# Kernel tuning notes

Hardware: AMD Instinct MI355X
Metric: run time of the kernel (lower is better)

The kernel has to match this reference:

```python
import jax, jax.numpy as jnp
import numpy as np

E, B, F, L = 4, 8192, 2048, 100  # envs, batch/env, feature dim, num classes
LAM = 1.0  # hparams['RERM_lam']


def setup_inputs() -> dict:
    key = jax.random.key(0)
    k1, k2, k3 = jax.random.split(key, 3)
    feats = jax.random.normal(k1, (E, B, F), jnp.float32)
    y = jax.random.randint(k2, (E, B), 0, L)
    W = jax.random.normal(k3, (F, L), jnp.float32) * 0.02
    b = jnp.zeros((L,), jnp.float32)
    return {"feats": feats, "y": y, "W": W, "b": b}


def _rerm_loss(feats, y, W, b):
    # --- per-(label, env) masked means (mean_table / visit_table) ---
    onehot = jax.nn.one_hot(y, L, dtype=feats.dtype)          # [E,B,L]
    counts = onehot.sum(axis=1)                               # [E,L]
    sums = jnp.einsum('ebl,ebf->elf', onehot, feats)          # [E,L,F]
    means = sums / jnp.maximum(counts, 1.0)[..., None]        # [E,L,F]
    visit = (counts > 0).astype(feats.dtype)                  # [E,L]

    # --- torch.var(mean_table[i, fetch_envs, :], dim=1): variance over
    # feature dim per env (unbiased, /(F-1)), then mean over visited envs ---
    mu = means.mean(axis=-1, keepdims=True)                   # [E,L,1]
    var = jnp.sum((means - mu) ** 2, axis=-1) / (F - 1)       # [E,L]

    nvis = visit.sum(axis=0)                                  # [L]
    sel = (nvis > 1.5).astype(feats.dtype)                    # labels with >1 env
    per_label = (var * visit).sum(axis=0) / jnp.maximum(nvis, 1.0)  # [L]
    nzlabel = jnp.maximum(sel.sum(), 1.0)
    mean_loss = LAM * jnp.sum(per_label * sel) / nzlabel

    # --- cross-entropy over all envs concatenated ---
    logits = feats.reshape(E * B, F) @ W + b                  # [E*B,L]
    logp = jax.nn.log_softmax(logits, axis=-1)
    ce = -jnp.take_along_axis(logp, y.reshape(-1, 1), axis=1).mean()

    return mean_loss + ce


def reference(feats, y, W, b):
    return _rerm_loss(feats, y, W, b)
```

## Files before the change

kernel.cpp:

```cpp
#include <hip/hip_runtime.h>
#include <hip/hip_bf16.h>
#include <math.h>

#define E 4
#define B 8192
#define F 2048
#define L 100
#define NROWS (E * B)
#define LAMBDA 1.0f

typedef __attribute__((ext_vector_type(8))) short bf16x8;
typedef __attribute__((ext_vector_type(4))) float f32x4;

static __device__ inline unsigned short f2bf(float x) {
    unsigned u = __float_as_uint(x);
    unsigned r = (u + 0x7FFFu + ((u >> 16) & 1u)) >> 16;
    return (unsigned short)r;
}

#define SG 4
#define NSG 25
#define SBS 8
#define SRW (B / SBS)
#define NSUM (E * SBS * NSG)

#define GBM 128
#define GNC 112
#define GKC 64
#define APAD 72
#define NGEMM (NROWS / GBM)

__global__ void __launch_bounds__(256) k_prep(const float* __restrict__ W,
                                              unsigned short* __restrict__ Wt) {
    int g = blockIdx.x * 256 + threadIdx.x;
    int n = g >> 9;
    int k = (g & 511) * 4;
    ushort4 v;
    if (n < L) {
        v.x = f2bf(W[(size_t)(k + 0) * L + n]);
        v.y = f2bf(W[(size_t)(k + 1) * L + n]);
        v.z = f2bf(W[(size_t)(k + 2) * L + n]);
        v.w = f2bf(W[(size_t)(k + 3) * L + n]);
    } else {
        v.x = v.y = v.z = v.w = 0;
    }
    *(ushort4*)&Wt[(size_t)n * F + k] = v;
}

__global__ void __launch_bounds__(512, 4) k_main(const float* __restrict__ feats,
                                                 const int* __restrict__ y,
                                                 const unsigned short* __restrict__ Wt,
                                                 const float* __restrict__ bias,
                                                 float* __restrict__ partial,
                                                 int* __restrict__ counts,
                                                 float* __restrict__ ce_accum) {
    __shared__ __align__(16) char sm[34624];
    int t = threadIdx.x;

    if (blockIdx.x < NGEMM) {
        unsigned short* As = (unsigned short*)sm;
        unsigned short* Ws = As + GBM * APAD;
        float* red = (float*)(sm + 34560);
        int wave = t >> 6, lane = t & 63;
        int quad = lane >> 4, l16 = lane & 15;
        size_t row0 = (size_t)blockIdx.x * GBM;

        f32x4 acc[7];
#pragma unroll
        for (int ct = 0; ct < 7; ++ct) acc[ct] = (f32x4){0.f, 0.f, 0.f, 0.f};

        int srow = t >> 2;
        int sq = t & 3;

        const float* aptr = feats + (row0 + srow) * (size_t)F + sq * 16;
        const unsigned short* wptr = Wt + (size_t)srow * F + sq * 16;

        float4 pa[4];
        uint4 pw[2];
#pragma unroll
        for (int i = 0; i < 4; ++i) pa[i] = ((const float4*)aptr)[i];
        if (srow < GNC) {
#pragma unroll
            for (int i = 0; i < 2; ++i) pw[i] = ((const uint4*)wptr)[i];
        }

        for (int k0 = 0; k0 < F; k0 += GKC) {
            bf16x8 o0, o1;
            o0[0] = f2bf(pa[0].x); o0[1] = f2bf(pa[0].y); o0[2] = f2bf(pa[0].z); o0[3] = f2bf(pa[0].w);
            o0[4] = f2bf(pa[1].x); o0[5] = f2bf(pa[1].y); o0[6] = f2bf(pa[1].z); o0[7] = f2bf(pa[1].w);
            o1[0] = f2bf(pa[2].x); o1[1] = f2bf(pa[2].y); o1[2] = f2bf(pa[2].z); o1[3] = f2bf(pa[2].w);
            o1[4] = f2bf(pa[3].x); o1[5] = f2bf(pa[3].y); o1[6] = f2bf(pa[3].z); o1[7] = f2bf(pa[3].w);
            *(bf16x8*)&As[srow * APAD + sq * 16] = o0;
            *(bf16x8*)&As[srow * APAD + sq * 16 + 8] = o1;
            if (srow < GNC) {
                *(uint4*)&Ws[srow * APAD + sq * 16] = pw[0];
                *(uint4*)&Ws[srow * APAD + sq * 16 + 8] = pw[1];
            }
            __syncthreads();

            if (k0 + GKC < F) {
                const float* ap = aptr + k0 + GKC;
                const unsigned short* wp = wptr + k0 + GKC;
#pragma unroll
                for (int i = 0; i < 4; ++i) pa[i] = ((const float4*)ap)[i];
                if (srow < GNC) {
#pragma unroll
                    for (int i = 0; i < 2; ++i) pw[i] = ((const uint4*)wp)[i];
                }
            }

#pragma unroll
            for (int ks = 0; ks < 2; ++ks) {
                bf16x8 bfr = *(const bf16x8*)&As[(wave * 16 + l16) * APAD + ks * 32 + quad * 8];
#pragma unroll
                for (int ct = 0; ct < 7; ++ct) {
                    bf16x8 af = *(const bf16x8*)&Ws[(ct * 16 + l16) * APAD + ks * 32 + quad * 8];
                    acc[ct] = __builtin_amdgcn_mfma_f32_16x16x32_bf16(af, bfr, acc[ct], 0, 0, 0);
                }
            }
            __syncthreads();
        }

        int grow = (int)row0 + wave * 16 + l16;
        int lab = y[grow];
        float vv[7][4];
        float vm = -1e30f;
#pragma unroll
        for (int ct = 0; ct < 7; ++ct) {
#pragma unroll
            for (int r = 0; r < 4; ++r) {
                int c = ct * 16 + quad * 4 + r;
                float bb = (c < L) ? bias[c] : 0.f;
                float v = acc[ct][r] + bb;
                vv[ct][r] = v;
                if (c < L) vm = fmaxf(vm, v);
            }
        }
        vm = fmaxf(vm, __shfl_xor(vm, 16));
        vm = fmaxf(vm, __shfl_xor(vm, 32));
        float se = 0.f, tv = 0.f;
#pragma unroll
        for (int ct = 0; ct < 7; ++ct) {
#pragma unroll
            for (int r = 0; r < 4; ++r) {
                int c = ct * 16 + quad * 4 + r;
                if (c < L) se += __expf(vv[ct][r] - vm);
                if (c == lab) tv = vv[ct][r];
            }
        }
        se += __shfl_xor(se, 16);
        se += __shfl_xor(se, 32);
        tv += __shfl_xor(tv, 16);
        tv += __shfl_xor(tv, 32);
        float ce = vm + __logf(se) - tv;
#pragma unroll
        for (int s = 1; s <= 8; s <<= 1) ce += __shfl_xor(ce, s);
        if (lane == 0) red[wave] = ce;
        __syncthreads();
        if (t == 0) {
            float v = 0.f;
#pragma unroll
            for (int w = 0; w < 8; ++w) v += red[w];
            atomicAdd(ce_accum, v);
        }
    } else {
        int* ys = (int*)sm;
        unsigned short (*lists)[SRW] = (unsigned short (*)[SRW])(sm + 4096);
        int* cnt = (int*)(sm + 4096 + 8192);
        int bi = blockIdx.x - NGEMM;
        int lg = bi % NSG;
        int bs = (bi / NSG) % SBS;
        int e  = bi / (NSG * SBS);
        int lab0 = lg * SG;

        if (t < SG) cnt[t] = 0;
        const int* yb = y + e * B + bs * SRW;
        ys[t] = yb[t];
        ys[t + 512] = yb[t + 512];
        __syncthreads();

        for (int r = t; r < SRW; r += 512) {
            int lb = ys[r] - lab0;
            if ((unsigned)lb < SG) {
                int p = atomicAdd(&cnt[lb], 1);
                lists[lb][p] = (unsigned short)r;
            }
        }
        __syncthreads();

        const float* fb = feats + ((size_t)e * B + (size_t)bs * SRW) * F + t * 4;
#pragma unroll
        for (int lb = 0; lb < SG; ++lb) {
            int n = cnt[lb];
            float4 a0 = make_float4(0.f, 0.f, 0.f, 0.f);
            float4 a1 = make_float4(0.f, 0.f, 0.f, 0.f);
            int i = 0;
            for (; i + 2 <= n; i += 2) {
                int r0 = lists[lb][i];
                int r1 = lists[lb][i + 1];
                float4 x0 = *(const float4*)(fb + (size_t)r0 * F);
                float4 x1 = *(const float4*)(fb + (size_t)r1 * F);
                a0.x += x0.x; a0.y += x0.y; a0.z += x0.z; a0.w += x0.w;
                a1.x += x1.x; a1.y += x1.y; a1.z += x1.z; a1.w += x1.w;
            }
            if (i < n) {
                int r0 = lists[lb][i];
                float4 x0 = *(const float4*)(fb + (size_t)r0 * F);
                a0.x += x0.x; a0.y += x0.y; a0.z += x0.z; a0.w += x0.w;
            }
            float4 s;
            s.x = a0.x + a1.x; s.y = a0.y + a1.y;
            s.z = a0.z + a1.z; s.w = a0.w + a1.w;
            *(float4*)&partial[(((size_t)e * SBS + bs) * L + lab0 + lb) * F + t * 4] = s;
        }
        if (t < SG) atomicAdd(&counts[e * L + lab0 + t], cnt[t]);
    }
}

__global__ void k_var(const float* __restrict__ partial,
                      const int* __restrict__ counts,
                      float* __restrict__ var_out) {
    int el = blockIdx.x;
    int e = el / L, l = el % L;
    int t = threadIdx.x;
    float inv = 1.f / fmaxf((float)counts[el], 1.f);
    float sm = 0.f, sm2 = 0.f;
    for (int f = t; f < F; f += 256) {
        float s = 0.f;
#pragma unroll
        for (int bs = 0; bs < SBS; ++bs)
            s += partial[(((size_t)e * SBS + bs) * L + l) * F + f];
        float m = s * inv;
        sm += m; sm2 += m * m;
    }
    __shared__ float r1[256], r2[256];
    r1[t] = sm; r2[t] = sm2;
    __syncthreads();
    for (int s = 128; s > 0; s >>= 1) {
        if (t < s) { r1[t] += r1[t + s]; r2[t] += r2[t + s]; }
        __syncthreads();
    }
    if (t == 0) {
        float S = r1[0], S2 = r2[0];
        var_out[el] = (S2 - S * S / (float)F) / (float)(F - 1);
    }
}

__global__ void k_final(const int* __restrict__ counts,
                        const float* __restrict__ var_in,
                        const float* __restrict__ ce_accum,
                        float* __restrict__ out) {
    __shared__ float s_sum[128], s_cnt[128];
    int t = threadIdx.x;
    float selsum = 0.f, selcnt = 0.f;
    for (int l = t; l < L; l += 128) {
        float nvis = 0.f, vsum = 0.f;
        for (int e = 0; e < E; ++e) {
            if (counts[e * L + l] > 0) { nvis += 1.f; vsum += var_in[e * L + l]; }
        }
        float per_label = vsum / fmaxf(nvis, 1.f);
        if (nvis > 1.5f) { selsum += per_label; selcnt += 1.f; }
    }
    s_sum[t] = selsum; s_cnt[t] = selcnt;
    __syncthreads();
    for (int s = 64; s > 0; s >>= 1) {
        if (t < s) { s_sum[t] += s_sum[t + s]; s_cnt[t] += s_cnt[t + s]; }
        __syncthreads();
    }
    if (t == 0) {
        float mean_loss = LAMBDA * s_sum[0] / fmaxf(s_cnt[0], 1.f);
        float ce = ce_accum[0] / (float)NROWS;
        out[0] = mean_loss + ce;
    }
}

extern "C" void kernel_launch(void* const* d_in, const int* in_sizes, int n_in,
                              void* d_out, int out_size, void* d_ws, size_t ws_size,
                              hipStream_t stream) {
    const float* feats = (const float*)d_in[0];
    const int*   y     = (const int*)d_in[1];
    const float* Wm    = (const float*)d_in[2];
    const float* bias  = (const float*)d_in[3];
    float* out = (float*)d_out;

    char* ws = (char*)d_ws;
    float*          ce_accum = (float*)ws;
    int*            counts   = (int*)(ws + 256);
    float*          var_buf  = (float*)(ws + 2048);
    float*          partial  = (float*)(ws + 4096);
    unsigned short* Wt       = (unsigned short*)(ws + 4096 + (size_t)E * SBS * L * F * 4);

    hipMemsetAsync(ce_accum, 0, sizeof(float), stream);
    hipMemsetAsync(counts, 0, E * L * sizeof(int), stream);

    k_prep<<<(GNC * 512) / 256, 256, 0, stream>>>(Wm, Wt);
    k_main<<<NGEMM + NSUM, 512, 0, stream>>>(feats, y, Wt, bias, partial, counts, ce_accum);
    k_var<<<E * L, 256, 0, stream>>>(partial, counts, var_buf);
    k_final<<<1, 128, 0, stream>>>(counts, var_buf, ce_accum, out);
}
```

Before: 438.3 us.

## Merge per-label gather lists and software-pipeline row loads; cheaper bf16 packing

The masked-sum blocks now keep one combined row list tagged with the label index instead of four separate lists. They walk it in groups of four, prefetching the next group's feature rows while the current group is accumulated into four per-label accumulators. This aims to raise memory-level parallelism and remove the serialized short per-label loops. Separately, the GEMM staging path converts fp32 to bf16 with a single add plus a byte permute per pair of values, which is cheaper than the old round-to-nearest-even helper. That packing rounds half-up rather than to even, and the combined list uses a second shared atomic counter.

```diff
diff --git a/kernel.cpp b/kernel.cpp
--- a/kernel.cpp
+++ b/kernel.cpp
@@ -47,6 +47,12 @@
     *(ushort4*)&Wt[(size_t)n * F + k] = v;
 }
 
+static __device__ inline unsigned pack_bf(float lo, float hi) {
+    unsigned ul = __float_as_uint(lo) + 0x8000u;
+    unsigned uh = __float_as_uint(hi) + 0x8000u;
+    return __builtin_amdgcn_perm(uh, ul, 0x07060302u);
+}
+
 __global__ void __launch_bounds__(512, 4) k_main(const float* __restrict__ feats,
                                                  const int* __restrict__ y,
                                                  const unsigned short* __restrict__ Wt,
@@ -85,13 +91,14 @@
         }
 
         for (int k0 = 0; k0 < F; k0 += GKC) {
-            bf16x8 o0, o1;
-            o0[0] = f2bf(pa[0].x); o0[1] = f2bf(pa[0].y); o0[2] = f2bf(pa[0].z); o0[3] = f2bf(pa[0].w);
-            o0[4] = f2bf(pa[1].x); o0[5] = f2bf(pa[1].y); o0[6] = f2bf(pa[1].z); o0[7] = f2bf(pa[1].w);
-            o1[0] = f2bf(pa[2].x); o1[1] = f2bf(pa[2].y); o1[2] = f2bf(pa[2].z); o1[3] = f2bf(pa[2].w);
-            o1[4] = f2bf(pa[3].x); o1[5] = f2bf(pa[3].y); o1[6] = f2bf(pa[3].z); o1[7] = f2bf(pa[3].w);
-            *(bf16x8*)&As[srow * APAD + sq * 16] = o0;
-            *(bf16x8*)&As[srow * APAD + sq * 16 + 8] = o1;
+            unsigned u[8];
+#pragma unroll
+            for (int i = 0; i < 4; ++i) {
+                u[i * 2]     = pack_bf(pa[i].x, pa[i].y);
+                u[i * 2 + 1] = pack_bf(pa[i].z, pa[i].w);
+            }
+            *(uint4*)&As[srow * APAD + sq * 16]     = make_uint4(u[0], u[1], u[2], u[3]);
+            *(uint4*)&As[srow * APAD + sq * 16 + 8] = make_uint4(u[4], u[5], u[6], u[7]);
             if (srow < GNC) {
                 *(uint4*)&Ws[srow * APAD + sq * 16] = pw[0];
                 *(uint4*)&Ws[srow * APAD + sq * 16 + 8] = pw[1];
@@ -165,15 +172,17 @@
         }
     } else {
         int* ys = (int*)sm;
-        unsigned short (*lists)[SRW] = (unsigned short (*)[SRW])(sm + 4096);
-        int* cnt = (int*)(sm + 4096 + 8192);
+        unsigned short* list = (unsigned short*)(sm + 4096);
+        int* cnt4 = (int*)(sm + 4096 + 2048);
+        int* ntot = (int*)(sm + 4096 + 2048 + 16);
         int bi = blockIdx.x - NGEMM;
         int lg = bi % NSG;
         int bs = (bi / NSG) % SBS;
         int e  = bi / (NSG * SBS);
         int lab0 = lg * SG;
 
-        if (t < SG) cnt[t] = 0;
+        if (t < SG) cnt4[t] = 0;
+        if (t == 8) ntot[0] = 0;
         const int* yb = y + e * B + bs * SRW;
         ys[t] = yb[t];
         ys[t + 512] = yb[t + 512];
@@ -182,38 +191,63 @@
         for (int r = t; r < SRW; r += 512) {
             int lb = ys[r] - lab0;
             if ((unsigned)lb < SG) {
-                int p = atomicAdd(&cnt[lb], 1);
-                lists[lb][p] = (unsigned short)r;
-            }
-        }
+                atomicAdd(&cnt4[lb], 1);
+                int p = atomicAdd(ntot, 1);
+                list[p] = (unsigned short)(r | (lb << 10));
+            }
+        }
+        __syncthreads();
+        int n = ntot[0];
+        int npad = (n + 3) & ~3;
+        if (t < npad - n) list[n + t] = 0;
         __syncthreads();
 
         const float* fb = feats + ((size_t)e * B + (size_t)bs * SRW) * F + t * 4;
-#pragma unroll
-        for (int lb = 0; lb < SG; ++lb) {
-            int n = cnt[lb];
-            float4 a0 = make_float4(0.f, 0.f, 0.f, 0.f);
-            float4 a1 = make_float4(0.f, 0.f, 0.f, 0.f);
-            int i = 0;
-            for (; i + 2 <= n; i += 2) {
-                int r0 = lists[lb][i];
-                int r1 = lists[lb][i + 1];
-                float4 x0 = *(const float4*)(fb + (size_t)r0 * F);
-                float4 x1 = *(const float4*)(fb + (size_t)r1 * F);
-                a0.x += x0.x; a0.y += x0.y; a0.z += x0.z; a0.w += x0.w;
-                a1.x += x1.x; a1.y += x1.y; a1.z += x1.z; a1.w += x1.w;
-            }
-            if (i < n) {
-                int r0 = lists[lb][i];
-                float4 x0 = *(const float4*)(fb + (size_t)r0 * F);
-                a0.x += x0.x; a0.y += x0.y; a0.z += x0.z; a0.w += x0.w;
-            }
-            float4 s;
-            s.x = a0.x + a1.x; s.y = a0.y + a1.y;
-            s.z = a0.z + a1.z; s.w = a0.w + a1.w;
-            *(float4*)&partial[(((size_t)e * SBS + bs) * L + lab0 + lb) * F + t * 4] = s;
-        }
-        if (t < SG) atomicAdd(&counts[e * L + lab0 + t], cnt[t]);
+        float4 a0 = make_float4(0.f, 0.f, 0.f, 0.f);
+        float4 a1 = a0, a2 = a0, a3 = a0;
+
+        float4 x[4];
+        int tg[4];
+        if (n > 0) {
+#pragma unroll
+            for (int j = 0; j < 4; ++j) {
+                int ev = list[j];
+                tg[j] = ev >> 10;
+                x[j] = *(const float4*)(fb + (size_t)(ev & 1023) * F);
+            }
+            for (int i = 0; i < npad; i += 4) {
+                float4 nx[4];
+                int ntg[4];
+                if (i + 4 < npad) {
+#pragma unroll
+                    for (int j = 0; j < 4; ++j) {
+                        int ev = list[i + 4 + j];
+                        ntg[j] = ev >> 10;
+                        nx[j] = *(const float4*)(fb + (size_t)(ev & 1023) * F);
+                    }
+                }
+#pragma unroll
+                for (int j = 0; j < 4; ++j) {
+                    if (i + j < n) {
+                        float4 v = x[j];
+                        int g = tg[j];
+                        if (g == 0)      { a0.x += v.x; a0.y += v.y; a0.z += v.z; a0.w += v.w; }
+                        else if (g == 1) { a1.x += v.x; a1.y += v.y; a1.z += v.z; a1.w += v.w; }
+                        else if (g == 2) { a2.x += v.x; a2.y += v.y; a2.z += v.z; a2.w += v.w; }
+                        else             { a3.x += v.x; a3.y += v.y; a3.z += v.z; a3.w += v.w; }
+                    }
+                }
+#pragma unroll
+                for (int j = 0; j < 4; ++j) { x[j] = nx[j]; tg[j] = ntg[j]; }
+            }
+        }
+
+        float* pb = partial + (((size_t)e * SBS + bs) * L + lab0) * F + t * 4;
+        *(float4*)(pb + 0 * F) = a0;
+        *(float4*)(pb + 1 * F) = a1;
+        *(float4*)(pb + 2 * F) = a2;
+        *(float4*)(pb + 3 * F) = a3;
+        if (t < SG) atomicAdd(&counts[e * L + lab0 + t], cnt4[t]);
     }
 }
 
```

Measured after the change: 435.7 us. Within noise of the previous version (-0.6%).
